# Kernel optimization log

Measured on AMD Instinct MI355X. Metric: run time of the kernel, lower is better.

The kernel has to match this reference:

```python
import jax, jax.numpy as jnp
import numpy as np
from jax import lax

H = 512      # hidden_size (== embed dim)
K = 128      # attr_size
V = 32000    # output_size (vocab)
ANUM = 20    # aspect_num = len(aspect_ids)//100
N, B = 64, 32
T, S, A = 256, 32, 5


def setup_inputs() -> dict:
    key = jax.random.key(0)
    ks = jax.random.split(key, 32)
    f = lambda i, shape, s=0.02: (jax.random.normal(ks[i], shape, jnp.float32) * s)
    inp = {
        "input_seq": jax.random.randint(ks[0], (N, B), 0, V, jnp.int32),
        "last_hidden": jax.random.normal(ks[1], (1, B, H), jnp.float32),
        "encoder_out1": jax.random.normal(ks[2], (T, B, H), jnp.float32),
        "encoder_out2": jax.random.normal(ks[3], (S, B, H), jnp.float32),
        "encoder_out3": jax.random.normal(ks[4], (A, B, K), jnp.float32),
        "encoder_out4": jax.random.normal(ks[5], (A, B, ANUM), jnp.float32),
        "aspect_ids": jax.random.randint(ks[6], (100 * ANUM,), 0, V, jnp.int32),
        # learned parameters
        "emb": f(7, (V, H)),
        "gru_Wih": f(8, (3 * H, H)), "gru_Whh": f(9, (3 * H, H)),
        "gru_bih": f(10, (3 * H,)), "gru_bhh": f(11, (3 * H,)),
        "attn_W": f(12, (H, 2 * H)), "attn_b": f(13, (H,)), "attn_v": f(14, (H,)),
        "attr_W": f(15, (H, H + K)), "attr_b": f(16, (H,)), "attr_v": f(17, (H,)),
        "concat_W": f(18, (H, 3 * H + K)), "concat_b": f(19, (H,)),
        "out_W": f(20, (V, H)), "out_b": f(21, (V,)),
        "gate_W": f(22, (ANUM, 2 * H + ANUM)), "gate_b": f(23, (ANUM,)),
        "proj_W": f(24, (ANUM, 2 * ANUM)), "proj_b": f(25, (ANUM,)),
    }
    return inp


def _gru(x, h0, Wih, Whh, bih, bhh):
    # x: (N,B,H); h0: (B,H). PyTorch gate order: reset, update, new.
    def step(h, xt):
        gi = xt @ Wih.T + bih
        gh = h @ Whh.T + bhh
        ir, iz, inn = jnp.split(gi, 3, axis=-1)
        hr, hz, hn = jnp.split(gh, 3, axis=-1)
        r = jax.nn.sigmoid(ir + hr)
        z = jax.nn.sigmoid(iz + hz)
        n = jnp.tanh(inn + r * hn)
        h_new = (1.0 - z) * n + z * h
        return h_new, h_new
    hT, ys = lax.scan(step, h0, x)
    return ys, hT


def _attn(hidden, enc, W, b, v):
    # Faithful to Attn/AttributeAttn: energies[b,n,t] = tanh(v . (W @ cat(hidden[n,b], enc[t,b]) + b))
    # W @ cat = hidden @ Wh^T + enc @ We^T; dot with v distributes -> avoid (T,N,B,*) blowup.
    Hh = hidden.shape[-1]
    Wh, We = W[:, :Hh], W[:, Hh:]
    a = hidden @ (Wh.T @ v) + jnp.dot(b, v)   # (N,B)
    c = enc @ (We.T @ v)                       # (T,B)
    e = jnp.tanh(a.T[:, :, None] + c.T[:, None, :])  # (B,N,T)
    return jax.nn.softmax(e, axis=2)


def reference(input_seq, last_hidden, encoder_out1, encoder_out2, encoder_out3,
              encoder_out4, aspect_ids, emb, gru_Wih, gru_Whh, gru_bih, gru_bhh,
              attn_W, attn_b, attn_v, attr_W, attr_b, attr_v, concat_W, concat_b,
              out_W, out_b, gate_W, gate_b, proj_W, proj_b):
    seq_len = input_seq.shape[0]
    embedded = emb[input_seq]                                   # (N,B,H), dropout=eval noop
    rnn_output, hT = _gru(embedded, last_hidden[0], gru_Wih, gru_Whh, gru_bih, gru_bhh)
    hidden = hT[None]                                           # (1,B,H)

    aw1 = _attn(rnn_output, encoder_out1, attn_W, attn_b, attn_v)   # (B,N,T)
    ctx1 = jnp.einsum('bnt,tbh->nbh', aw1, encoder_out1)
    aw2 = _attn(rnn_output, encoder_out2, attn_W, attn_b, attn_v)   # (B,N,S)
    ctx2 = jnp.einsum('bns,sbh->nbh', aw2, encoder_out2)
    aw3 = _attn(rnn_output, encoder_out3, attr_W, attr_b, attr_v)   # (B,N,A)
    ctx3 = jnp.einsum('bna,abk->nbk', aw3, encoder_out3)

    concat_input = jnp.concatenate([rnn_output, ctx1, ctx2, ctx3], axis=2)
    concat_output = jnp.tanh(concat_input @ concat_W.T + concat_b)  # (N,B,H)
    output = concat_output @ out_W.T + out_b                        # (N,B,V)

    e4 = jnp.concatenate([encoder_out4[0], encoder_out4[1]], axis=-1)  # (B,2*ANUM)
    e4 = e4 @ proj_W.T + proj_b                                        # (B,ANUM)
    e4 = jnp.broadcast_to(e4[None], (seq_len,) + e4.shape)             # (N,B,ANUM)

    gate = jnp.tanh(jnp.concatenate([embedded, rnn_output, e4], axis=2) @ gate_W.T + gate_b)
    vals = jnp.tile(gate, (1, 1, 100))                                 # (N,B,100*ANUM)
    output = output.at[:, :, aspect_ids].add(vals)
    return output, hidden, aw1, aw2, aw3, gate
```

## Files before the change

kernel.cpp:

```cpp
#include <hip/hip_runtime.h>
#include <hip/hip_bf16.h>

#define HDIM 512
#define KA   128
#define VOC  32000
#define ANUMC 20
#define NSEQ 64
#define BATCH 32
#define TLEN 256
#define SLEN 32
#define ALEN 5
#define NB   2048
#define CIN  1664
#define G3H  1536
#define GB   64

typedef __bf16 bf16;
typedef bf16 v8bf __attribute__((ext_vector_type(8)));
typedef float v4f __attribute__((ext_vector_type(4)));

#define DEV __device__ __forceinline__

DEV float sigmoidf_(float x) { return 1.f / (1.f + expf(-x)); }

__global__ void k_zero(int* bar) {
  for (int i = threadIdx.x; i < GB * 32; i += 256) bar[i] = 0;
}

__global__ void k_init0(float* addtab, int* colnz) {
  int i = blockIdx.x * 256 + threadIdx.x;
  if (i < VOC * ANUMC) addtab[i] = 0.f;
  if (i < VOC) colnz[i] = 0;
}
__global__ void k_init1(const int* __restrict__ ids, float* addtab, int* colnz) {
  for (int k = threadIdx.x; k < 2000; k += 256) {
    int j = ids[k];
    atomicAdd(addtab + (size_t)j * ANUMC + (k % ANUMC), 1.0f);
    colnz[j] = 1;
  }
}

__global__ void k_vec(const float* __restrict__ attn_W, const float* __restrict__ attn_b,
                      const float* __restrict__ attn_v,
                      const float* __restrict__ attr_W, const float* __restrict__ attr_b,
                      const float* __restrict__ attr_v,
                      const float* __restrict__ enc4, const float* __restrict__ pW,
                      const float* __restrict__ pb, float* __restrict__ misc) {
  int tid = threadIdx.x;
  int blk = blockIdx.x;
  if (blk == 0) {
    for (int i = tid; i < 512; i += 256) {
      float s = 0.f;
      for (int j = 0; j < 512; ++j) s += attn_W[j * 1024 + i] * attn_v[j];
      misc[i] = s;
    }
  } else if (blk == 1) {
    for (int i = tid; i < 512; i += 256) {
      float s = 0.f;
      for (int j = 0; j < 512; ++j) s += attn_W[j * 1024 + 512 + i] * attn_v[j];
      misc[512 + i] = s;
    }
  } else if (blk == 2) {
    for (int i = tid; i < 512; i += 256) {
      float s = 0.f;
      for (int j = 0; j < 512; ++j) s += attr_W[j * 640 + i] * attr_v[j];
      misc[1024 + i] = s;
    }
  } else {
    for (int i = tid; i < 128; i += 256) {
      float s = 0.f;
      for (int j = 0; j < 512; ++j) s += attr_W[j * 640 + 512 + i] * attr_v[j];
      misc[1536 + i] = s;
    }
    if (tid == 128) {
      float s = 0.f;
      for (int j = 0; j < 512; ++j) s += attn_b[j] * attn_v[j];
      misc[1664] = s;
    }
    if (tid == 129) {
      float s = 0.f;
      for (int j = 0; j < 512; ++j) s += attr_b[j] * attr_v[j];
      misc[1665] = s;
    }
    for (int i = tid; i < BATCH * ANUMC; i += 256) {
      int b = i / ANUMC, j = i % ANUMC;
      float s = pb[j];
      for (int q = 0; q < ANUMC; ++q) s += pW[j * 40 + q] * enc4[b * ANUMC + q];
      for (int q = 0; q < ANUMC; ++q) s += pW[j * 40 + 20 + q] * enc4[BATCH * ANUMC + b * ANUMC + q];
      misc[1792 + i] = s;
    }
  }
}

__global__ void k_embcvt(const int* __restrict__ seq, const float* __restrict__ emb,
                         float* __restrict__ embedded, bf16* __restrict__ emb_bf,
                         const float* __restrict__ Wih, bf16* __restrict__ Wih_bf,
                         const float* __restrict__ cW, bf16* __restrict__ cW_bf,
                         const float* __restrict__ oW, bf16* __restrict__ oW_bf) {
  size_t i = (size_t)blockIdx.x * 256 + threadIdx.x;
  const size_t s0 = 1048576, s1 = s0 + 786432, s2 = s1 + 851968, s3 = s2 + 16384000;
  if (i < s0) {
    int row = (int)(i >> 9), col = (int)(i & 511);
    float v = emb[(size_t)seq[row] * 512 + col];
    embedded[i] = v;
    emb_bf[i] = (bf16)v;
  } else if (i < s1) {
    size_t j = i - s0;
    Wih_bf[j] = (bf16)Wih[j];
  } else if (i < s2) {
    size_t j = i - s1;
    cW_bf[j] = (bf16)cW[j];
  } else if (i < s3) {
    size_t j = i - s2;
    oW_bf[j] = (bf16)oW[j];
  }
}

__global__ void k_c(const float* __restrict__ enc1, const float* __restrict__ enc2,
                    const float* __restrict__ enc3, float* __restrict__ misc) {
  int i = blockIdx.x * 256 + threadIdx.x;
  const float* u1e = misc + 512;
  const float* u3e = misc + 1536;
  if (i < 8192) {
    const float* row = enc1 + (size_t)i * 512;
    float s = 0.f;
#pragma unroll 4
    for (int j = 0; j < 512; j += 4) {
      float4 a = *(const float4*)(row + j);
      float4 u = *(const float4*)(u1e + j);
      s += a.x * u.x + a.y * u.y + a.z * u.z + a.w * u.w;
    }
    misc[2560 + i] = s;
  } else if (i < 8192 + 1024) {
    int k = i - 8192;
    const float* row = enc2 + (size_t)k * 512;
    float s = 0.f;
#pragma unroll 4
    for (int j = 0; j < 512; j += 4) {
      float4 a = *(const float4*)(row + j);
      float4 u = *(const float4*)(u1e + j);
      s += a.x * u.x + a.y * u.y + a.z * u.z + a.w * u.w;
    }
    misc[10752 + k] = s;
  } else if (i < 8192 + 1024 + 160) {
    int k = i - 9216;
    const float* row = enc3 + (size_t)k * 128;
    float s = 0.f;
#pragma unroll 4
    for (int j = 0; j < 128; j += 4) {
      float4 a = *(const float4*)(row + j);
      float4 u = *(const float4*)(u3e + j);
      s += a.x * u.x + a.y * u.y + a.z * u.z + a.w * u.w;
    }
    misc[11776 + k] = s;
  }
}

template <int EPI>
__global__ __launch_bounds__(256) void k_gemm_bt(const bf16* __restrict__ A,
                                                 const bf16* __restrict__ Bm,
                                                 const float* __restrict__ bias,
                                                 float* __restrict__ Cf, bf16* __restrict__ Cb,
                                                 int M, int Nn, int Kd,
                                                 const float* __restrict__ addtab,
                                                 const int* __restrict__ colnz,
                                                 const float* __restrict__ gate) {
  __shared__ __align__(16) unsigned short As[128 * 64];
  __shared__ __align__(16) unsigned short Bs[128 * 64];
  int tid = threadIdx.x;
  int m0 = blockIdx.y * 128;
  int n0 = blockIdx.x * 128;
  int lane = tid & 63;
  int wv = tid >> 6;
  int wm = wv & 1, wn = wv >> 1;
  int l15 = lane & 15, quad = lane >> 4;
  int srow = tid >> 3;
  int sch = tid & 7;

  v4f acc[4][4];
#pragma unroll
  for (int i = 0; i < 4; ++i)
#pragma unroll
    for (int j = 0; j < 4; ++j) acc[i][j] = (v4f){0.f, 0.f, 0.f, 0.f};

  for (int kb = 0; kb < Kd; kb += 64) {
#pragma unroll
    for (int r = 0; r < 4; ++r) {
      int row = r * 32 + srow;
      uint4 va = *(const uint4*)(A + (size_t)(m0 + row) * Kd + kb + sch * 8);
      *(uint4*)((char*)As + row * 128 + ((sch ^ (row & 7)) << 4)) = va;
      uint4 vb = *(const uint4*)(Bm + (size_t)(n0 + row) * Kd + kb + sch * 8);
      *(uint4*)((char*)Bs + row * 128 + ((sch ^ (row & 7)) << 4)) = vb;
    }
    __syncthreads();
#pragma unroll
    for (int ks = 0; ks < 2; ++ks) {
      v8bf af[4], bfr[4];
      int c = ks * 4 + quad;
#pragma unroll
      for (int i = 0; i < 4; ++i) {
        int mr = wm * 64 + i * 16 + l15;
        af[i] = *(const v8bf*)((const char*)As + mr * 128 + ((c ^ (mr & 7)) << 4));
      }
#pragma unroll
      for (int j = 0; j < 4; ++j) {
        int nr = wn * 64 + j * 16 + l15;
        bfr[j] = *(const v8bf*)((const char*)Bs + nr * 128 + ((c ^ (nr & 7)) << 4));
      }
#pragma unroll
      for (int i = 0; i < 4; ++i)
#pragma unroll
        for (int j = 0; j < 4; ++j)
          acc[i][j] = __builtin_amdgcn_mfma_f32_16x16x32_bf16(af[i], bfr[j], acc[i][j], 0, 0, 0);
    }
    __syncthreads();
  }
#pragma unroll
  for (int i = 0; i < 4; ++i) {
    int gr0 = m0 + wm * 64 + i * 16 + quad * 4;
#pragma unroll
    for (int j = 0; j < 4; ++j) {
      int gc = n0 + wn * 64 + j * 16 + l15;
      float bs = bias[gc];
      if (EPI == 2) {
        int nz = colnz[gc];
        float ar[ANUMC];
        if (nz) {
#pragma unroll
          for (int a = 0; a < ANUMC; ++a) ar[a] = addtab[(size_t)gc * ANUMC + a];
        }
#pragma unroll
        for (int reg = 0; reg < 4; ++reg) {
          float v = acc[i][j][reg] + bs;
          if (nz) {
            const float* gr = gate + (size_t)(gr0 + reg) * ANUMC;
#pragma unroll
            for (int a = 0; a < ANUMC; ++a) v += ar[a] * gr[a];
          }
          Cf[(size_t)(gr0 + reg) * Nn + gc] = v;
        }
      } else {
#pragma unroll
        for (int reg = 0; reg < 4; ++reg) {
          float v = acc[i][j][reg] + bs;
          if (EPI == 1)
            Cb[(size_t)(gr0 + reg) * Nn + gc] = (bf16)tanhf(v);
          else
            Cf[(size_t)(gr0 + reg) * Nn + gc] = v;
        }
      }
    }
  }
}

__global__ __launch_bounds__(256) void k_gru(const float* __restrict__ gi,
                                             const float* __restrict__ Whh,
                                             const float* __restrict__ bhh,
                                             const float* __restrict__ lasth,
                                             float* __restrict__ rnn,
                                             bf16* __restrict__ concat_bf,
                                             unsigned long long* __restrict__ hx,
                                             int* __restrict__ bar) {
  struct SMEM {
    unsigned short hs[32 * 512];
    float gh[32 * 29];
    unsigned short hnew[256];
    int go;
  };
  __shared__ __align__(16) SMEM sm;
  int tid = threadIdx.x;
  int blk = blockIdx.x;
  int c0 = blk * 8;

  int lane = tid & 63;
  int w = tid >> 6;
  int l15 = lane & 15, quad = lane >> 4;
  int m0 = (w & 1) * 16;
  int n0 = (w >> 1) * 16;

  if (tid == 0) sm.go = 0;

  v8bf breg[16];
  {
    int nr = n0 + l15;
    if (nr > 23) nr = 23;
    const float* wrow = Whh + (size_t)((nr >> 3) * 512 + c0 + (nr & 7)) * 512;
#pragma unroll
    for (int it = 0; it < 16; ++it) {
      int k0 = it * 32 + quad * 8;
      float4 x = *(const float4*)(wrow + k0);
      float4 y = *(const float4*)(wrow + k0 + 4);
      v8bf vv;
      vv[0] = (bf16)x.x; vv[1] = (bf16)x.y; vv[2] = (bf16)x.z; vv[3] = (bf16)x.w;
      vv[4] = (bf16)y.x; vv[5] = (bf16)y.y; vv[6] = (bf16)y.z; vv[7] = (bf16)y.w;
      breg[it] = vv;
    }
  }

#pragma unroll
  for (int rnd = 0; rnd < 8; ++rnd) {
    int ch = rnd * 256 + tid;
    int bb = ch >> 6, cc = ch & 63;
    const float* hp = lasth + bb * 512 + cc * 8;
    float4 x = *(const float4*)hp;
    float4 y = *(const float4*)(hp + 4);
    v8bf vv;
    vv[0] = (bf16)x.x; vv[1] = (bf16)x.y; vv[2] = (bf16)x.z; vv[3] = (bf16)x.w;
    vv[4] = (bf16)y.x; vv[5] = (bf16)y.y; vv[6] = (bf16)y.z; vv[7] = (bf16)y.w;
    *(v8bf*)((char*)sm.hs + bb * 1024 + ((cc ^ (bb & 7)) << 4)) = vv;
  }

  int cb = tid >> 3, j = tid & 7, c = c0 + j;
  float hprev = lasth[cb * 512 + c];
  float b_r = bhh[c], b_z = bhh[512 + c], b_n = bhh[1024 + c];
  __syncthreads();

  for (int t = 0; t < 64; ++t) {
    const float* gii = gi + ((size_t)t * 32 + cb) * G3H;
    float g_r = gii[c];
    float g_z = gii[512 + c];
    float g_n = gii[1024 + c];

    {
      v4f acc0 = (v4f){0.f, 0.f, 0.f, 0.f};
      v4f acc1 = (v4f){0.f, 0.f, 0.f, 0.f};
      int mr = m0 + l15;
#pragma unroll
      for (int it = 0; it < 8; ++it) {
        {
          int ccx = it * 4 + quad;
          v8bf af = *(const v8bf*)((const char*)sm.hs + mr * 1024 + ((ccx ^ (mr & 7)) << 4));
          acc0 = __builtin_amdgcn_mfma_f32_16x16x32_bf16(af, breg[it], acc0, 0, 0, 0);
        }
        {
          int ccx = (it + 8) * 4 + quad;
          v8bf af = *(const v8bf*)((const char*)sm.hs + mr * 1024 + ((ccx ^ (mr & 7)) << 4));
          acc1 = __builtin_amdgcn_mfma_f32_16x16x32_bf16(af, breg[it + 8], acc1, 0, 0, 0);
        }
      }
      v4f acc = acc0 + acc1;
      if (n0 == 0 || l15 < 8) {
#pragma unroll
        for (int reg = 0; reg < 4; ++reg)
          sm.gh[(m0 + quad * 4 + reg) * 29 + n0 + l15] = acc[reg];
      }
    }
    __syncthreads();

    {
      float ar = sm.gh[cb * 29 + j] + b_r;
      float az = sm.gh[cb * 29 + 8 + j] + b_z;
      float an = sm.gh[cb * 29 + 16 + j] + b_n;
      float rg = sigmoidf_(g_r + ar);
      float zg = sigmoidf_(g_z + az);
      float ng = tanhf(g_n + rg * an);
      float hn = (1.f - zg) * ng + zg * hprev;
      hprev = hn;
      rnn[((size_t)t * 32 + cb) * 512 + c] = hn;
      bf16 hb = (bf16)hn;
      concat_bf[((size_t)t * 32 + cb) * CIN + c] = hb;
      sm.hnew[tid] = *(unsigned short*)&hb;
    }

    if (t < 63) {
      __syncthreads();
      int target = t + 1;
      int pnext = target & 1;
      if (w == 0) {
        unsigned long long pk = *(const unsigned long long*)(sm.hnew + lane * 4);
        int wd = (lane >> 1) * 128 + blk * 2 + (lane & 1);
        __hip_atomic_store(hx + (size_t)pnext * 4096 + wd, pk,
                           __ATOMIC_RELAXED, __HIP_MEMORY_SCOPE_AGENT);
        asm volatile("s_waitcnt vmcnt(0)" ::: "memory");
        if (lane == 0)
          __hip_atomic_store(&bar[blk * 32], target, __ATOMIC_RELAXED,
                             __HIP_MEMORY_SCOPE_AGENT);
        for (;;) {
          int v = __hip_atomic_load(&bar[lane * 32], __ATOMIC_RELAXED,
                                    __HIP_MEMORY_SCOPE_AGENT);
          if (__all(v >= target)) break;
          __builtin_amdgcn_s_sleep(1);
        }
        if (lane == 0) *(volatile int*)&sm.go = target;
      } else {
        while (*(volatile int*)&sm.go < target) __builtin_amdgcn_s_sleep(1);
      }

      {
        const unsigned long long* src = hx + (size_t)pnext * 4096 + w * 1024 + lane;
        unsigned long long vv[16];
#pragma unroll
        for (int i = 0; i < 16; ++i)
          vv[i] = __hip_atomic_load(src + i * 64, __ATOMIC_RELAXED,
                                    __HIP_MEMORY_SCOPE_AGENT);
#pragma unroll
        for (int i = 0; i < 16; ++i) {
          int W = w * 1024 + i * 64 + lane;
          int bb = W >> 7, wr = W & 127;
          int u = wr >> 1, half = wr & 1;
          *(unsigned long long*)((char*)sm.hs + bb * 1024 +
                                 (((u ^ (bb & 7)) << 4) | (half << 3))) = vv[i];
        }
      }
      __syncthreads();
    }
  }
}

__global__ __launch_bounds__(256) void k_attnrow(const float* __restrict__ rnn,
                                                 const float* __restrict__ misc,
                                                 float* __restrict__ aw1,
                                                 float* __restrict__ aw2,
                                                 float* __restrict__ aw3) {
  int wv = (blockIdx.x * 256 + threadIdx.x) >> 6;
  int lane = threadIdx.x & 63;
  if (wv >= 2048) return;
  int n = wv >> 5, b = wv & 31;
  const float* u1a = misc;
  const float* u3h = misc + 1024;
  const float* c1 = misc + 2560;
  const float* c2 = misc + 10752;
  const float* c3 = misc + 11776;
  const float* row = rnn + (size_t)(n * 32 + b) * 512;
  float s1 = 0.f, s3 = 0.f;
#pragma unroll
  for (int q = 0; q < 8; ++q) {
    int j = lane * 8 + q;
    float rv = row[j];
    s1 += rv * u1a[j];
    s3 += rv * u3h[j];
  }
  for (int o = 32; o > 0; o >>= 1) {
    s1 += __shfl_down(s1, o);
    s3 += __shfl_down(s3, o);
  }
  s1 = __shfl(s1, 0) + misc[1664];
  s3 = __shfl(s3, 0) + misc[1665];

  float e[4];
  float mx = -1e30f;
#pragma unroll
  for (int q = 0; q < 4; ++q) {
    int t = q * 64 + lane;
    e[q] = tanhf(s1 + c1[t * 32 + b]);
    mx = fmaxf(mx, e[q]);
  }
  for (int o = 32; o > 0; o >>= 1) mx = fmaxf(mx, __shfl_xor(mx, o));
  float sum = 0.f;
#pragma unroll
  for (int q = 0; q < 4; ++q) {
    e[q] = expf(e[q] - mx);
    sum += e[q];
  }
  for (int o = 32; o > 0; o >>= 1) sum += __shfl_xor(sum, o);
  float inv = 1.f / sum;
  size_t base1 = (size_t)(b * 64 + n) * 256;
#pragma unroll
  for (int q = 0; q < 4; ++q) aw1[base1 + q * 64 + lane] = e[q] * inv;

  float e2 = (lane < 32) ? tanhf(s1 + c2[lane * 32 + b]) : -1e30f;
  float m2 = e2;
  for (int o = 32; o > 0; o >>= 1) m2 = fmaxf(m2, __shfl_xor(m2, o));
  float x2 = (lane < 32) ? expf(e2 - m2) : 0.f;
  float sm2 = x2;
  for (int o = 32; o > 0; o >>= 1) sm2 += __shfl_xor(sm2, o);
  if (lane < 32) aw2[(size_t)(b * 64 + n) * 32 + lane] = x2 / sm2;

  float e3 = (lane < 5) ? tanhf(s3 + c3[lane * 32 + b]) : -1e30f;
  float m3 = e3;
  for (int o = 32; o > 0; o >>= 1) m3 = fmaxf(m3, __shfl_xor(m3, o));
  float x3 = (lane < 5) ? expf(e3 - m3) : 0.f;
  float sm3 = x3;
  for (int o = 32; o > 0; o >>= 1) sm3 += __shfl_xor(sm3, o);
  if (lane < 5) aw3[(size_t)(b * 64 + n) * 5 + lane] = x3 / sm3;
}

template <int TL, int COFF>
__global__ __launch_bounds__(256) void k_ctx(const float* __restrict__ aw,
                                             const float* __restrict__ enc,
                                             bf16* __restrict__ concat_bf) {
  __shared__ __align__(16) float awsT[TL * 36];
  int tid = threadIdx.x;
  int bx = blockIdx.x;
  int b = bx >> 2, q = (bx >> 1) & 1, nh = bx & 1;
  for (int i = tid; i < 32 * TL; i += 256) {
    int n = i / TL, te = i % TL;
    awsT[te * 36 + n] = aw[(size_t)b * 64 * TL + (size_t)(nh * 32 + n) * TL + te];
  }
  __syncthreads();
  int col = q * 256 + tid;
  float4 acc[8];
#pragma unroll
  for (int n4 = 0; n4 < 8; ++n4) acc[n4] = make_float4(0.f, 0.f, 0.f, 0.f);
  for (int te = 0; te < TL; ++te) {
    float v = enc[((size_t)te * 32 + b) * 512 + col];
#pragma unroll
    for (int n4 = 0; n4 < 8; ++n4) {
      float4 wv = *(const float4*)(awsT + te * 36 + n4 * 4);
      acc[n4].x += wv.x * v;
      acc[n4].y += wv.y * v;
      acc[n4].z += wv.z * v;
      acc[n4].w += wv.w * v;
    }
  }
#pragma unroll
  for (int n4 = 0; n4 < 8; ++n4) {
    int ng = nh * 32 + n4 * 4;
    concat_bf[((size_t)(ng + 0) * 32 + b) * CIN + COFF + col] = (bf16)acc[n4].x;
    concat_bf[((size_t)(ng + 1) * 32 + b) * CIN + COFF + col] = (bf16)acc[n4].y;
    concat_bf[((size_t)(ng + 2) * 32 + b) * CIN + COFF + col] = (bf16)acc[n4].z;
    concat_bf[((size_t)(ng + 3) * 32 + b) * CIN + COFF + col] = (bf16)acc[n4].w;
  }
}

__global__ void k_ctx3_misc(const float* __restrict__ aw3, const float* __restrict__ enc3,
                            const float* __restrict__ rnn, bf16* __restrict__ concat_bf,
                            float* __restrict__ hid) {
  int i = blockIdx.x * 256 + threadIdx.x;
  if (i < NB * 128) {
    int row = i >> 7, k = i & 127;
    int n = row >> 5, b = row & 31;
    float s = 0.f;
#pragma unroll
    for (int a = 0; a < 5; ++a)
      s += aw3[(size_t)(b * 64 + n) * 5 + a] * enc3[((size_t)a * 32 + b) * 128 + k];
    concat_bf[(size_t)row * CIN + 1536 + k] = (bf16)s;
  } else {
    int j = i - NB * 128;
    if (j < 16384) hid[j] = rnn[(size_t)63 * 16384 + j];
  }
}

__global__ __launch_bounds__(256) void k_gate(const float* __restrict__ embedded,
                                              const float* __restrict__ rnn,
                                              const float* __restrict__ misc,
                                              const float* __restrict__ gW,
                                              const float* __restrict__ gb,
                                              float* __restrict__ gate) {
  int i = blockIdx.x * 256 + threadIdx.x;
  if (i >= NB * ANUMC) return;
  int row = i / ANUMC, j = i % ANUMC;
  int b = row & 31;
  const float* w = gW + (size_t)j * 1044;
  const float* e = embedded + (size_t)row * 512;
  const float* r = rnn + (size_t)row * 512;
  float s = gb[j];
#pragma unroll 4
  for (int k = 0; k < 512; k += 4) {
    float4 a = *(const float4*)(e + k);
    float4 ww = *(const float4*)(w + k);
    s += a.x * ww.x + a.y * ww.y + a.z * ww.z + a.w * ww.w;
  }
#pragma unroll 4
  for (int k = 0; k < 512; k += 4) {
    float4 a = *(const float4*)(r + k);
    float4 ww = *(const float4*)(w + 512 + k);
    s += a.x * ww.x + a.y * ww.y + a.z * ww.z + a.w * ww.w;
  }
  const float* e4 = misc + 1792 + b * ANUMC;
#pragma unroll
  for (int q = 0; q < ANUMC; ++q) s += w[1024 + q] * e4[q];
  gate[i] = tanhf(s);
}

extern "C" void kernel_launch(void* const* d_in, const int* in_sizes, int n_in,
                              void* d_out, int out_size, void* d_ws, size_t ws_size,
                              hipStream_t stream) {
  const int* seq = (const int*)d_in[0];
  const float* lasth = (const float*)d_in[1];
  const float* enc1 = (const float*)d_in[2];
  const float* enc2 = (const float*)d_in[3];
  const float* enc3 = (const float*)d_in[4];
  const float* enc4 = (const float*)d_in[5];
  const int* aspect = (const int*)d_in[6];
  const float* emb = (const float*)d_in[7];
  const float* Wih = (const float*)d_in[8];
  const float* Whh = (const float*)d_in[9];
  const float* bih = (const float*)d_in[10];
  const float* bhh = (const float*)d_in[11];
  const float* attn_W = (const float*)d_in[12];
  const float* attn_b = (const float*)d_in[13];
  const float* attn_v = (const float*)d_in[14];
  const float* attr_W = (const float*)d_in[15];
  const float* attr_b = (const float*)d_in[16];
  const float* attr_v = (const float*)d_in[17];
  const float* cW = (const float*)d_in[18];
  const float* cbias = (const float*)d_in[19];
  const float* oW = (const float*)d_in[20];
  const float* ob = (const float*)d_in[21];
  const float* gW = (const float*)d_in[22];
  const float* gb = (const float*)d_in[23];
  const float* pW = (const float*)d_in[24];
  const float* pb = (const float*)d_in[25];

  char* ws = (char*)d_ws;
  float* misc = (float*)(ws + 0);
  float* embedded = (float*)(ws + 65536);
  float* gi = (float*)(ws + 4259840);
  float* rnn = (float*)(ws + 16842752);
  bf16* emb_bf = (bf16*)(ws + 21037056);
  bf16* Wih_bf = (bf16*)(ws + 23134208);
  bf16* cW_bf = (bf16*)(ws + 24707072);
  bf16* oW_bf = (bf16*)(ws + 26411008);
  bf16* concat_bf = (bf16*)(ws + 59179008);
  bf16* cout_bf = (bf16*)(ws + 65994752);
  unsigned long long* hx = (unsigned long long*)(ws + 68091904);
  int* bar = (int*)(misc + 12032);
  float* addtab = (float*)(ws + 4259840);
  int* colnz = (int*)(ws + 4259840 + 2560000);

  float* out = (float*)d_out;
  float* hid_out = out + 65536000;
  float* aw1 = out + 65552384;
  float* aw2 = out + 66076672;
  float* aw3 = out + 66142208;
  float* gate = out + 66152448;

  k_zero<<<1, 256, 0, stream>>>(bar);
  k_vec<<<4, 256, 0, stream>>>(attn_W, attn_b, attn_v, attr_W, attr_b, attr_v, enc4, pW, pb, misc);
  k_embcvt<<<74496, 256, 0, stream>>>(seq, emb, embedded, emb_bf, Wih, Wih_bf, cW, cW_bf, oW,
                                      oW_bf);
  k_c<<<37, 256, 0, stream>>>(enc1, enc2, enc3, misc);
  k_gemm_bt<0><<<dim3(12, 16), 256, 0, stream>>>(emb_bf, Wih_bf, bih, gi, nullptr, NB, G3H, 512,
                                                 nullptr, nullptr, nullptr);
  k_gru<<<GB, 256, 0, stream>>>(gi, Whh, bhh, lasth, rnn, concat_bf, hx, bar);
  k_init0<<<2625, 256, 0, stream>>>(addtab, colnz);
  k_init1<<<1, 256, 0, stream>>>(aspect, addtab, colnz);
  k_attnrow<<<512, 256, 0, stream>>>(rnn, misc, aw1, aw2, aw3);
  k_ctx<256, 512><<<128, 256, 0, stream>>>(aw1, enc1, concat_bf);
  k_ctx<32, 1024><<<128, 256, 0, stream>>>(aw2, enc2, concat_bf);
  k_ctx3_misc<<<1088, 256, 0, stream>>>(aw3, enc3, rnn, concat_bf, hid_out);
  k_gate<<<160, 256, 0, stream>>>(embedded, rnn, misc, gW, gb, gate);
  k_gemm_bt<1><<<dim3(4, 16), 256, 0, stream>>>(concat_bf, cW_bf, cbias, nullptr, cout_bf, NB,
                                                512, CIN, nullptr, nullptr, nullptr);
  k_gemm_bt<2><<<dim3(250, 16), 256, 0, stream>>>(cout_bf, oW_bf, ob, out, nullptr, NB, VOC, 512,
                                                  addtab, colnz, gate);
}
```

Measured before the change: 1.089 ms.

## Use direct global-to-LDS loads and XCD-aware tile remapping in bf16 GEMM

The GEMM tile loads now use global_load_lds builtins that write straight into shared memory. The XOR swizzle is applied on the global source column, so tiles no longer pass through registers. The 2D grid becomes a 1D grid with a block-id remap that spreads consecutive tiles across the 8 XCDs, iterating M-tiles fastest within an N column so B-matrix rows are reused in cache. Launch bounds now request two blocks per CU. It relies on the compiler inserting the right vmcnt waits before the barrier for the LDS DMA.

New measurement: 1.050 ms. -3.5%, faster.

```diff
diff --git a/kernel.cpp b/kernel.cpp
--- a/kernel.cpp
+++ b/kernel.cpp
@@ -157,25 +157,29 @@
 }
 
 template <int EPI>
-__global__ __launch_bounds__(256) void k_gemm_bt(const bf16* __restrict__ A,
-                                                 const bf16* __restrict__ Bm,
-                                                 const float* __restrict__ bias,
-                                                 float* __restrict__ Cf, bf16* __restrict__ Cb,
-                                                 int M, int Nn, int Kd,
-                                                 const float* __restrict__ addtab,
-                                                 const int* __restrict__ colnz,
-                                                 const float* __restrict__ gate) {
+__global__ __launch_bounds__(256, 2) void k_gemm_bt(const bf16* __restrict__ A,
+                                                    const bf16* __restrict__ Bm,
+                                                    const float* __restrict__ bias,
+                                                    float* __restrict__ Cf, bf16* __restrict__ Cb,
+                                                    int M, int Nn, int Kd,
+                                                    const float* __restrict__ addtab,
+                                                    const int* __restrict__ colnz,
+                                                    const float* __restrict__ gate) {
   __shared__ __align__(16) unsigned short As[128 * 64];
   __shared__ __align__(16) unsigned short Bs[128 * 64];
   int tid = threadIdx.x;
-  int m0 = blockIdx.y * 128;
-  int n0 = blockIdx.x * 128;
+  int nwg = gridDim.x;
+  int cpx = nwg >> 3;
+  int wgid = (blockIdx.x & 7) * cpx + (blockIdx.x >> 3);
+  int MT = M >> 7;
+  int m0 = (wgid % MT) << 7;
+  int n0 = (wgid / MT) << 7;
   int lane = tid & 63;
   int wv = tid >> 6;
   int wm = wv & 1, wn = wv >> 1;
   int l15 = lane & 15, quad = lane >> 4;
-  int srow = tid >> 3;
-  int sch = tid & 7;
+  int l8r = lane >> 3;
+  int lp = lane & 7;
 
   v4f acc[4][4];
 #pragma unroll
@@ -186,11 +190,15 @@
   for (int kb = 0; kb < Kd; kb += 64) {
 #pragma unroll
     for (int r = 0; r < 4; ++r) {
-      int row = r * 32 + srow;
-      uint4 va = *(const uint4*)(A + (size_t)(m0 + row) * Kd + kb + sch * 8);
-      *(uint4*)((char*)As + row * 128 + ((sch ^ (row & 7)) << 4)) = va;
-      uint4 vb = *(const uint4*)(Bm + (size_t)(n0 + row) * Kd + kb + sch * 8);
-      *(uint4*)((char*)Bs + row * 128 + ((sch ^ (row & 7)) << 4)) = vb;
+      int g = wv * 4 + r;
+      int lr = g * 8 + l8r;
+      int ca = (lp ^ (lr & 7)) * 8;
+      __builtin_amdgcn_global_load_lds(
+          (const __attribute__((address_space(1))) void*)(A + (size_t)(m0 + lr) * Kd + kb + ca),
+          (__attribute__((address_space(3))) void*)((char*)As + g * 1024), 16, 0, 0);
+      __builtin_amdgcn_global_load_lds(
+          (const __attribute__((address_space(1))) void*)(Bm + (size_t)(n0 + lr) * Kd + kb + ca),
+          (__attribute__((address_space(3))) void*)((char*)Bs + g * 1024), 16, 0, 0);
     }
     __syncthreads();
 #pragma unroll
@@ -621,8 +629,8 @@
   k_embcvt<<<74496, 256, 0, stream>>>(seq, emb, embedded, emb_bf, Wih, Wih_bf, cW, cW_bf, oW,
                                       oW_bf);
   k_c<<<37, 256, 0, stream>>>(enc1, enc2, enc3, misc);
-  k_gemm_bt<0><<<dim3(12, 16), 256, 0, stream>>>(emb_bf, Wih_bf, bih, gi, nullptr, NB, G3H, 512,
-                                                 nullptr, nullptr, nullptr);
+  k_gemm_bt<0><<<192, 256, 0, stream>>>(emb_bf, Wih_bf, bih, gi, nullptr, NB, G3H, 512,
+                                        nullptr, nullptr, nullptr);
   k_gru<<<GB, 256, 0, stream>>>(gi, Whh, bhh, lasth, rnn, concat_bf, hx, bar);
   k_init0<<<2625, 256, 0, stream>>>(addtab, colnz);
   k_init1<<<1, 256, 0, stream>>>(aspect, addtab, colnz);
@@ -631,8 +639,8 @@
   k_ctx<32, 1024><<<128, 256, 0, stream>>>(aw2, enc2, concat_bf);
   k_ctx3_misc<<<1088, 256, 0, stream>>>(aw3, enc3, rnn, concat_bf, hid_out);
   k_gate<<<160, 256, 0, stream>>>(embedded, rnn, misc, gW, gb, gate);
-  k_gemm_bt<1><<<dim3(4, 16), 256, 0, stream>>>(concat_bf, cW_bf, cbias, nullptr, cout_bf, NB,
-                                                512, CIN, nullptr, nullptr, nullptr);
-  k_gemm_bt<2><<<dim3(250, 16), 256, 0, stream>>>(cout_bf, oW_bf, ob, out, nullptr, NB, VOC, 512,
-                                                  addtab, colnz, gate);
-}
+  k_gemm_bt<1><<<64, 256, 0, stream>>>(concat_bf, cW_bf, cbias, nullptr, cout_bf, NB,
+                                       512, CIN, nullptr, nullptr, nullptr);
+  k_gemm_bt<2><<<4000, 256, 0, stream>>>(cout_bf, oW_bf, ob, out, nullptr, NB, VOC, 512,
+                                         addtab, colnz, gate);
+}
```
